# Kernel tuning notes

Measured on AMD Instinct MI355X. Metric: run time of the kernel, lower is better.

The kernel has to match this reference:

```python
import jax, jax.numpy as jnp
import numpy as np


def _block_causal_mask(cu_seqlens, seq_len):
    """Boolean [seq_len, seq_len] mask: True = attend (same doc AND causal)."""
    positions = jnp.arange(seq_len)
    # searchsorted(side='right') - 1 maps each position to its document id
    seq_ids = jnp.searchsorted(cu_seqlens, positions, side='right') - 1
    same_seq = seq_ids[:, None] == seq_ids[None, :]
    causal = positions[None, :] <= positions[:, None]
    return same_seq & causal


def setup_inputs() -> dict:
    key = jax.random.key(0)
    kq, kk, kv, kc = jax.random.split(key, 4)
    B, H, S, D = 1, 16, 4096, 128
    q = jax.random.normal(kq, (B, H, S, D), dtype=jnp.float32)
    k = jax.random.normal(kk, (B, H, S, D), dtype=jnp.float32)
    v = jax.random.normal(kv, (B, H, S, D), dtype=jnp.float32)
    # 8 packed documents: interior boundaries are sorted random ints in (0, S)
    inner = jnp.sort(jax.random.randint(kc, (7,), 1, S, dtype=jnp.int64))
    cu_seqlens = jnp.concatenate([
        jnp.zeros((1,), jnp.int64), inner, jnp.full((1,), S, jnp.int64)
    ])
    return {"q": q, "k": k, "v": v, "cu_seqlens": cu_seqlens, "max_seqlen": S}


def reference(q, k, v, cu_seqlens, max_seqlen):
    # q, k, v: [B, H, S, D]; block-diagonal causal SDPA over packed sequences.
    S, D = q.shape[2], q.shape[3]
    scale = 1.0 / jnp.sqrt(jnp.asarray(D, q.dtype))
    allow = _block_causal_mask(cu_seqlens, S)  # [S, S] bool
    scores = jnp.einsum('bhsd,bhtd->bhst', q, k) * scale  # [B, H, S, S]
    neg_inf = jnp.asarray(-jnp.inf, scores.dtype)
    scores = jnp.where(allow[None, None], scores, neg_inf)
    probs = jax.nn.softmax(scores, axis=-1)
    return jnp.einsum('bhst,bhtd->bhsd', probs, v)
```

## Files before the change

kernel.cpp:

```cpp
#include <hip/hip_runtime.h>

typedef float  f32x4  __attribute__((ext_vector_type(4)));
typedef __bf16 bf16x8 __attribute__((ext_vector_type(8)));
typedef unsigned short u16;
typedef u16 u16x8 __attribute__((ext_vector_type(8)));
typedef u16 u16x4 __attribute__((ext_vector_type(4)));

#define HEADS 16
#define DIM   128
#define QT    64
#define KTILE 64
#define PSTR  72
#define KSTR  136
#define VSTR  68

__device__ __forceinline__ u16 f2bf(float f) {
    unsigned u = __builtin_bit_cast(unsigned, f);
    u += 0x7FFFu + ((u >> 16) & 1u);
    return (u16)(u >> 16);
}

__device__ __forceinline__ void dma16(const void* g, void* l) {
    auto* gp = (const __attribute__((address_space(1))) unsigned*)(uintptr_t)g;
    auto* lp = (__attribute__((address_space(3))) unsigned*)(uintptr_t)l;
    __builtin_amdgcn_global_load_lds(gp, lp, 16, 0, 0);
}

__global__ __launch_bounds__(256) void prep_k(
    const float* __restrict__ K, u16* __restrict__ KB, int S, int total)
{
    int t = blockIdx.x * 256 + threadIdx.x;
    if (t >= total) return;
    int g = t & 15;
    int k = (t >> 4) % S;
    int h = (t >> 4) / S;
    int r = k & 63, tile = k >> 6;
    const float* src = K + ((long)(h * S + k) * DIM + g * 8);
    f32x4 a = *(const f32x4*)src;
    f32x4 b = *(const f32x4*)(src + 4);
    u16x8 o;
    o[0]=f2bf(a[0]); o[1]=f2bf(a[1]); o[2]=f2bf(a[2]); o[3]=f2bf(a[3]);
    o[4]=f2bf(b[0]); o[5]=f2bf(b[1]); o[6]=f2bf(b[2]); o[7]=f2bf(b[3]);
    long tb = (long)(h * (S >> 6) + tile) * 8192;
    *(u16x8*)&KB[tb + r * 128 + ((g ^ (r & 7)) << 3)] = o;
}

__global__ __launch_bounds__(256) void prep_v(
    const float* __restrict__ V, u16* __restrict__ VB, int S)
{
    __shared__ __align__(16) u16 T[128 * 72];
    int nt = S >> 6;
    int tile = blockIdx.x % nt, h = blockIdx.x / nt;
    int t = threadIdx.x;
    int col4 = (t & 31) * 4;
    int row  = t >> 5;
    const float* src = V + ((long)(h * S + tile * 64)) * DIM;
#pragma unroll
    for (int it = 0; it < 8; ++it) {
        int k = row + it * 8;
        f32x4 x = *(const f32x4*)(src + (long)k * DIM + col4);
        T[(col4 + 0) * 72 + k] = f2bf(x[0]);
        T[(col4 + 1) * 72 + k] = f2bf(x[1]);
        T[(col4 + 2) * 72 + k] = f2bf(x[2]);
        T[(col4 + 3) * 72 + k] = f2bf(x[3]);
    }
    __syncthreads();
    long tb = (long)(h * nt + tile) * 8192;
#pragma unroll
    for (int it = 0; it < 4; ++it) {
        int idx = t + it * 256;
        int d = idx >> 3, g2 = idx & 7;
        u16x8 o = *(const u16x8*)&T[d * 72 + g2 * 8];
        *(u16x8*)&VB[tb + d * 64 + ((g2 ^ (d & 7)) << 3)] = o;
    }
}

__global__ __launch_bounds__(256, 3) void fa_main(
    const float* __restrict__ Q, const u16* __restrict__ KB,
    const u16* __restrict__ VB, const void* __restrict__ cu_raw,
    int n_cu, float* __restrict__ O, int S, int n_qb)
{
    __shared__ __align__(16) u16 Kb[64 * 128];
    __shared__ __align__(16) u16 Vt[144 * 64];
    __shared__ __align__(16) u16 Pw[4][16 * PSTR];
    __shared__ int cu_s[32];

    const int tid  = threadIdx.x;
    const int wave = tid >> 6, lane = tid & 63;
    const int quad = lane >> 4, l16 = lane & 15;
    const int h  = blockIdx.x & (HEADS - 1);
    const int qb = (n_qb - 1) - (blockIdx.x >> 4);
    const int q0 = qb * QT;

    {
        const int* cu32 = (const int*)cu_raw;
        bool is64 = (cu32[1] == 0);
        for (int t = tid; t < n_cu; t += blockDim.x)
            cu_s[t] = is64 ? (int)((const long long*)cu_raw)[t] : cu32[t];
    }
    for (int i = tid; i < 1024; i += 256)
        Vt[8192 + i] = (i < 64) ? (u16)0x3F80 : (u16)0;
    __syncthreads();

    const float sc2 = 0.08838834764831845f * 1.4426950408889634f;
    const long hb = (long)h * S * DIM;
    const long hk = (long)h * (S >> 6) * 8192;
    const int qend = q0 + QT;

    int qstart[4];
#pragma unroll
    for (int r = 0; r < 4; ++r) {
        int qi = q0 + wave * 16 + quad * 4 + r;
        int st = 0;
        for (int j = 0; j < n_cu; ++j) if (cu_s[j] <= qi) st = cu_s[j];
        qstart[r] = st;
    }
    int q0s = 0;
    for (int j = 0; j < n_cu; ++j) if (cu_s[j] <= q0) q0s = cu_s[j];

    bf16x8 qfrag[4];
    {
        const float* qp = Q + hb + (long)(q0 + wave * 16 + l16) * DIM + quad * 8;
#pragma unroll
        for (int kk = 0; kk < 4; ++kk) {
            f32x4 x = *(const f32x4*)(qp + kk * 32);
            f32x4 y = *(const f32x4*)(qp + kk * 32 + 4);
            u16x8 u;
            u[0]=f2bf(x[0]); u[1]=f2bf(x[1]); u[2]=f2bf(x[2]); u[3]=f2bf(x[3]);
            u[4]=f2bf(y[0]); u[5]=f2bf(y[1]); u[6]=f2bf(y[2]); u[7]=f2bf(y[3]);
            qfrag[kk] = __builtin_bit_cast(bf16x8, u);
        }
    }

    f32x4 acc[9];
#pragma unroll
    for (int dt = 0; dt < 9; ++dt) acc[dt] = (f32x4){0.f, 0.f, 0.f, 0.f};

    for (int kt = q0s & ~(KTILE - 1); kt < qend; kt += KTILE) {
        __syncthreads();
        {
            const u16* ks = KB + hk + (long)(kt >> 6) * 8192;
            const u16* vs = VB + hk + (long)(kt >> 6) * 8192;
#pragma unroll
            for (int c = 0; c < 4; ++c) {
                int ch = wave * 4 + c;
                dma16(ks + ch * 512 + lane * 8, &Kb[ch * 512]);
                dma16(vs + ch * 512 + lane * 8, &Vt[ch * 512]);
            }
        }
        __syncthreads();

        f32x4 sc[4];
#pragma unroll
        for (int nt = 0; nt < 4; ++nt) sc[nt] = (f32x4){0.f, 0.f, 0.f, 0.f};
#pragma unroll
        for (int kk = 0; kk < 4; ++kk)
#pragma unroll
            for (int nt = 0; nt < 4; ++nt) {
                int row = nt * 16 + l16;
                int g = kk * 4 + quad;
                u16x8 bu = *(const u16x8*)&Kb[row * 128 + ((g ^ (row & 7)) << 3)];
                sc[nt] = __builtin_amdgcn_mfma_f32_16x16x32_bf16(
                    qfrag[kk], __builtin_bit_cast(bf16x8, bu), sc[nt], 0, 0, 0);
            }

#pragma unroll
        for (int nt = 0; nt < 4; ++nt) {
            int kj = kt + nt * 16 + l16;
#pragma unroll
            for (int r = 0; r < 4; ++r) {
                int qi = q0 + wave * 16 + quad * 4 + r;
                bool ok = (kj >= qstart[r]) && (kj <= qi);
                float pv = ok ? __builtin_amdgcn_exp2f(sc[nt][r] * sc2) : 0.f;
                Pw[wave][(quad*4 + r) * PSTR + ((nt ^ quad) * 16 + l16)] = f2bf(pv);
            }
        }

#pragma unroll
        for (int kk2 = 0; kk2 < 2; ++kk2) {
            int colx = (kk2*32 + quad*8) ^ ((l16 >> 2) << 4);
            u16x8 au = *(const u16x8*)&Pw[wave][l16 * PSTR + colx];
            bf16x8 ap = __builtin_bit_cast(bf16x8, au);
#pragma unroll
            for (int dt = 0; dt < 9; ++dt) {
                int d = dt * 16 + l16;
                int g2 = kk2 * 4 + quad;
                u16x8 bu = *(const u16x8*)&Vt[(d << 6) + ((g2 ^ (d & 7)) << 3)];
                acc[dt] = __builtin_amdgcn_mfma_f32_16x16x32_bf16(
                    ap, __builtin_bit_cast(bf16x8, bu), acc[dt], 0, 0, 0);
            }
        }
    }

#pragma unroll
    for (int r = 0; r < 4; ++r) {
        float l = __shfl(acc[8][r], (lane & 48), 64);
        int qi = q0 + wave * 16 + quad * 4 + r;
        float inv = 1.f / l;
        float* op = O + hb + (long)qi * DIM + l16;
#pragma unroll
        for (int dt = 0; dt < 8; ++dt)
            op[dt * 16] = acc[dt][r] * inv;
    }
}

__global__ __launch_bounds__(256, 2) void fa_fallback(
    const float* __restrict__ Q, const float* __restrict__ K,
    const float* __restrict__ V, const void* __restrict__ cu_raw,
    int n_cu, float* __restrict__ O, int S)
{
    __shared__ __align__(16) u16 Kb[KTILE * KSTR];
    __shared__ __align__(16) u16 Vt[DIM * VSTR];
    __shared__ __align__(16) u16 Pw[4][16 * PSTR];
    __shared__ int cu_s[32];

    const int tid  = threadIdx.x;
    const int wave = tid >> 6, lane = tid & 63;
    const int quad = lane >> 4, l16 = lane & 15;
    const int q0   = blockIdx.x * QT;
    const int h    = blockIdx.y;
    const int cg = tid & 31, rr = tid >> 5;
    const int dv = tid & 127, hiv = tid >> 7;

    {
        const int* cu32 = (const int*)cu_raw;
        bool is64 = (cu32[1] == 0);
        for (int t = tid; t < n_cu; t += blockDim.x)
            cu_s[t] = is64 ? (int)((const long long*)cu_raw)[t] : cu32[t];
    }
    __syncthreads();

    const long hb = (long)h * S * DIM;
    const float NEG_INF = -__builtin_inff();
    const float scale = 0.08838834764831845f;

    int qstart[4];
#pragma unroll
    for (int r = 0; r < 4; ++r) {
        int qi = q0 + wave * 16 + quad * 4 + r;
        int st = 0;
        for (int j = 0; j < n_cu; ++j) if (cu_s[j] <= qi) st = cu_s[j];
        qstart[r] = st;
    }
    int q0s = 0;
    for (int j = 0; j < n_cu; ++j) if (cu_s[j] <= q0) q0s = cu_s[j];

    bf16x8 qfrag[4];
    {
        const float* qp = Q + hb + (long)(q0 + wave * 16 + l16) * DIM + quad * 8;
#pragma unroll
        for (int kk = 0; kk < 4; ++kk) {
            f32x4 x = *(const f32x4*)(qp + kk * 32);
            f32x4 y = *(const f32x4*)(qp + kk * 32 + 4);
            u16x8 u;
            u[0]=f2bf(x[0]); u[1]=f2bf(x[1]); u[2]=f2bf(x[2]); u[3]=f2bf(x[3]);
            u[4]=f2bf(y[0]); u[5]=f2bf(y[1]); u[6]=f2bf(y[2]); u[7]=f2bf(y[3]);
            qfrag[kk] = __builtin_bit_cast(bf16x8, u);
        }
    }

    f32x4 acc[8];
#pragma unroll
    for (int dt = 0; dt < 8; ++dt) acc[dt] = (f32x4){0.f, 0.f, 0.f, 0.f};
    float m_r[4], l_r[4];
#pragma unroll
    for (int r = 0; r < 4; ++r) { m_r[r] = NEG_INF; l_r[r] = 0.f; }

    for (int kt = q0s & ~(KTILE - 1); kt < q0 + QT; kt += KTILE) {
        __syncthreads();
        {
#pragma unroll
            for (int it = 0; it < 8; ++it) {
                f32x4 kx = *(const f32x4*)(K + hb + (long)(kt + rr + it*8) * DIM + cg*4);
                u16x4 kb4;
                kb4[0]=f2bf(kx[0]); kb4[1]=f2bf(kx[1]);
                kb4[2]=f2bf(kx[2]); kb4[3]=f2bf(kx[3]);
                *(u16x4*)&Kb[(rr + it*8) * KSTR + cg*4] = kb4;
            }
#pragma unroll
            for (int p = 0; p < 8; ++p) {
                int kq = 2*p + hiv;
                const float* vp = V + hb + (long)(kt + kq*4) * DIM + dv;
                u16x4 w;
                w[0]=f2bf(vp[0]); w[1]=f2bf(vp[(long)DIM]);
                w[2]=f2bf(vp[(long)2*DIM]); w[3]=f2bf(vp[(long)3*DIM]);
                *(u16x4*)&Vt[dv * VSTR + kq*4] = w;
            }
        }
        __syncthreads();

        f32x4 sc[4];
#pragma unroll
        for (int nt = 0; nt < 4; ++nt) sc[nt] = (f32x4){0.f, 0.f, 0.f, 0.f};
#pragma unroll
        for (int kk = 0; kk < 4; ++kk)
#pragma unroll
            for (int nt = 0; nt < 4; ++nt) {
                u16x8 bu = *(const u16x8*)&Kb[(nt*16 + l16) * KSTR + kk*32 + quad*8];
                sc[nt] = __builtin_amdgcn_mfma_f32_16x16x32_bf16(
                    qfrag[kk], __builtin_bit_cast(bf16x8, bu), sc[nt], 0, 0, 0);
            }
#pragma unroll
        for (int nt = 0; nt < 4; ++nt) {
            int kj = kt + nt * 16 + l16;
#pragma unroll
            for (int r = 0; r < 4; ++r) {
                int qi = q0 + wave * 16 + quad * 4 + r;
                bool ok = (kj >= qstart[r]) && (kj <= qi);
                sc[nt][r] = ok ? sc[nt][r] * scale : NEG_INF;
            }
        }
        float mnew[4], alpha[4], rsum[4];
#pragma unroll
        for (int r = 0; r < 4; ++r) {
            float tm = fmaxf(fmaxf(sc[0][r], sc[1][r]), fmaxf(sc[2][r], sc[3][r]));
#pragma unroll
            for (int off = 1; off < 16; off <<= 1)
                tm = fmaxf(tm, __shfl_xor(tm, off, 64));
            float mn = fmaxf(m_r[r], tm);
            mnew[r]  = mn;
            alpha[r] = (mn == NEG_INF) ? 1.f : __expf(m_r[r] - mn);
            rsum[r]  = 0.f;
        }
#pragma unroll
        for (int nt = 0; nt < 4; ++nt)
#pragma unroll
            for (int r = 0; r < 4; ++r) {
                float pv = (sc[nt][r] == NEG_INF) ? 0.f : __expf(sc[nt][r] - mnew[r]);
                sc[nt][r] = pv;
                rsum[r] += pv;
            }
#pragma unroll
        for (int r = 0; r < 4; ++r) {
            float s = rsum[r];
#pragma unroll
            for (int off = 1; off < 16; off <<= 1) s += __shfl_xor(s, off, 64);
            l_r[r] = l_r[r] * alpha[r] + s;
            m_r[r] = mnew[r];
        }
#pragma unroll
        for (int dt = 0; dt < 8; ++dt)
#pragma unroll
            for (int r = 0; r < 4; ++r) acc[dt][r] *= alpha[r];

#pragma unroll
        for (int nt = 0; nt < 4; ++nt)
#pragma unroll
            for (int r = 0; r < 4; ++r)
                Pw[wave][(quad*4 + r) * PSTR + ((nt ^ quad) * 16 + l16)] = f2bf(sc[nt][r]);

#pragma unroll
        for (int kk2 = 0; kk2 < 2; ++kk2) {
            int colx = (kk2*32 + quad*8) ^ ((l16 >> 2) << 4);
            u16x8 au = *(const u16x8*)&Pw[wave][l16 * PSTR + colx];
            bf16x8 ap = __builtin_bit_cast(bf16x8, au);
#pragma unroll
            for (int dt = 0; dt < 8; ++dt) {
                int base = (dt*16 + l16) * VSTR + kk2*32 + quad*8;
                u16x4 lo = *(const u16x4*)&Vt[base];
                u16x4 hi = *(const u16x4*)&Vt[base + 4];
                u16x8 bu;
                bu[0]=lo[0]; bu[1]=lo[1]; bu[2]=lo[2]; bu[3]=lo[3];
                bu[4]=hi[0]; bu[5]=hi[1]; bu[6]=hi[2]; bu[7]=hi[3];
                acc[dt] = __builtin_amdgcn_mfma_f32_16x16x32_bf16(
                    ap, __builtin_bit_cast(bf16x8, bu), acc[dt], 0, 0, 0);
            }
        }
    }

#pragma unroll
    for (int r = 0; r < 4; ++r) {
        int qi = q0 + wave * 16 + quad * 4 + r;
        float inv = 1.f / l_r[r];
        float* op = O + hb + (long)qi * DIM + l16;
#pragma unroll
        for (int dt = 0; dt < 8; ++dt)
            op[dt * 16] = acc[dt][r] * inv;
    }
}

extern "C" void kernel_launch(void* const* d_in, const int* in_sizes, int n_in,
                              void* d_out, int out_size, void* d_ws, size_t ws_size,
                              hipStream_t stream) {
    const float* q = (const float*)d_in[0];
    const float* k = (const float*)d_in[1];
    const float* v = (const float*)d_in[2];
    const void* cu = d_in[3];
    int n_cu = in_sizes[3];
    int S = in_sizes[0] / (HEADS * DIM);
    size_t perMat = (size_t)HEADS * S * 256;
    if (ws_size >= 2 * perMat) {
        u16* KB = (u16*)d_ws;
        u16* VB = (u16*)((char*)d_ws + perMat);
        int totalK = HEADS * S * 16;
        prep_k<<<dim3((totalK + 255) / 256), 256, 0, stream>>>(k, KB, S, totalK);
        prep_v<<<dim3(HEADS * (S >> 6)), 256, 0, stream>>>(v, VB, S);
        int n_qb = S / QT;
        fa_main<<<dim3(n_qb * HEADS), 256, 0, stream>>>(
            q, KB, VB, cu, n_cu, (float*)d_out, S, n_qb);
    } else {
        fa_fallback<<<dim3(S / QT, HEADS), 256, 0, stream>>>(
            q, k, v, cu, n_cu, (float*)d_out, S);
    }
}
```

Measured before the change: 188.0 us.

## Double query tile per block so each wave reuses K/V fragments over two row tiles

The main kernel's query tile grows from 64 to 128 rows, with each wave now handling two 16-row M-tiles. Each K fragment and V fragment read from LDS feeds two MFMAs, which halves LDS and global K/V traffic per query row. In exchange, register pressure roughly doubles, the occupancy bound drops from 3 to 2 blocks per CU, and there are half as many blocks with coarser causal tiles, so more masked work. The fallback kernel is pinned to 64-row tiles.

```diff
diff --git a/kernel.cpp b/kernel.cpp
--- a/kernel.cpp
+++ b/kernel.cpp
@@ -8,7 +8,7 @@
 
 #define HEADS 16
 #define DIM   128
-#define QT    64
+#define QT    128
 #define KTILE 64
 #define PSTR  72
 #define KSTR  136
@@ -75,14 +75,14 @@
     }
 }
 
-__global__ __launch_bounds__(256, 3) void fa_main(
+__global__ __launch_bounds__(256, 2) void fa_main(
     const float* __restrict__ Q, const u16* __restrict__ KB,
     const u16* __restrict__ VB, const void* __restrict__ cu_raw,
     int n_cu, float* __restrict__ O, int S, int n_qb)
 {
     __shared__ __align__(16) u16 Kb[64 * 128];
     __shared__ __align__(16) u16 Vt[144 * 64];
-    __shared__ __align__(16) u16 Pw[4][16 * PSTR];
+    __shared__ __align__(16) u16 Pw[4][32 * PSTR];
     __shared__ int cu_s[32];
 
     const int tid  = threadIdx.x;
@@ -91,6 +91,7 @@
     const int h  = blockIdx.x & (HEADS - 1);
     const int qb = (n_qb - 1) - (blockIdx.x >> 4);
     const int q0 = qb * QT;
+    const int wrow = q0 + wave * 32;
 
     {
         const int* cu32 = (const int*)cu_raw;
@@ -107,20 +108,23 @@
     const long hk = (long)h * (S >> 6) * 8192;
     const int qend = q0 + QT;
 
-    int qstart[4];
-#pragma unroll
-    for (int r = 0; r < 4; ++r) {
-        int qi = q0 + wave * 16 + quad * 4 + r;
-        int st = 0;
-        for (int j = 0; j < n_cu; ++j) if (cu_s[j] <= qi) st = cu_s[j];
-        qstart[r] = st;
-    }
+    int qstart[2][4];
+#pragma unroll
+    for (int mt = 0; mt < 2; ++mt)
+#pragma unroll
+        for (int r = 0; r < 4; ++r) {
+            int qi = wrow + mt * 16 + quad * 4 + r;
+            int st = 0;
+            for (int j = 0; j < n_cu; ++j) if (cu_s[j] <= qi) st = cu_s[j];
+            qstart[mt][r] = st;
+        }
     int q0s = 0;
     for (int j = 0; j < n_cu; ++j) if (cu_s[j] <= q0) q0s = cu_s[j];
 
-    bf16x8 qfrag[4];
-    {
-        const float* qp = Q + hb + (long)(q0 + wave * 16 + l16) * DIM + quad * 8;
+    bf16x8 qfrag[2][4];
+#pragma unroll
+    for (int mt = 0; mt < 2; ++mt) {
+        const float* qp = Q + hb + (long)(wrow + mt * 16 + l16) * DIM + quad * 8;
 #pragma unroll
         for (int kk = 0; kk < 4; ++kk) {
             f32x4 x = *(const f32x4*)(qp + kk * 32);
@@ -128,13 +132,15 @@
             u16x8 u;
             u[0]=f2bf(x[0]); u[1]=f2bf(x[1]); u[2]=f2bf(x[2]); u[3]=f2bf(x[3]);
             u[4]=f2bf(y[0]); u[5]=f2bf(y[1]); u[6]=f2bf(y[2]); u[7]=f2bf(y[3]);
-            qfrag[kk] = __builtin_bit_cast(bf16x8, u);
-        }
-    }
-
-    f32x4 acc[9];
-#pragma unroll
-    for (int dt = 0; dt < 9; ++dt) acc[dt] = (f32x4){0.f, 0.f, 0.f, 0.f};
+            qfrag[mt][kk] = __builtin_bit_cast(bf16x8, u);
+        }
+    }
+
+    f32x4 acc[2][9];
+#pragma unroll
+    for (int mt = 0; mt < 2; ++mt)
+#pragma unroll
+        for (int dt = 0; dt < 9; ++dt) acc[mt][dt] = (f32x4){0.f, 0.f, 0.f, 0.f};
 
     for (int kt = q0s & ~(KTILE - 1); kt < qend; kt += KTILE) {
         __syncthreads();
@@ -150,9 +156,11 @@
         }
         __syncthreads();
 
-        f32x4 sc[4];
-#pragma unroll
-        for (int nt = 0; nt < 4; ++nt) sc[nt] = (f32x4){0.f, 0.f, 0.f, 0.f};
+        f32x4 sc[2][4];
+#pragma unroll
+        for (int mt = 0; mt < 2; ++mt)
+#pragma unroll
+            for (int nt = 0; nt < 4; ++nt) sc[mt][nt] = (f32x4){0.f, 0.f, 0.f, 0.f};
 #pragma unroll
         for (int kk = 0; kk < 4; ++kk)
 #pragma unroll
@@ -160,48 +168,61 @@
                 int row = nt * 16 + l16;
                 int g = kk * 4 + quad;
                 u16x8 bu = *(const u16x8*)&Kb[row * 128 + ((g ^ (row & 7)) << 3)];
-                sc[nt] = __builtin_amdgcn_mfma_f32_16x16x32_bf16(
-                    qfrag[kk], __builtin_bit_cast(bf16x8, bu), sc[nt], 0, 0, 0);
-            }
-
-#pragma unroll
-        for (int nt = 0; nt < 4; ++nt) {
-            int kj = kt + nt * 16 + l16;
-#pragma unroll
-            for (int r = 0; r < 4; ++r) {
-                int qi = q0 + wave * 16 + quad * 4 + r;
-                bool ok = (kj >= qstart[r]) && (kj <= qi);
-                float pv = ok ? __builtin_amdgcn_exp2f(sc[nt][r] * sc2) : 0.f;
-                Pw[wave][(quad*4 + r) * PSTR + ((nt ^ quad) * 16 + l16)] = f2bf(pv);
-            }
-        }
+                bf16x8 bf = __builtin_bit_cast(bf16x8, bu);
+                sc[0][nt] = __builtin_amdgcn_mfma_f32_16x16x32_bf16(
+                    qfrag[0][kk], bf, sc[0][nt], 0, 0, 0);
+                sc[1][nt] = __builtin_amdgcn_mfma_f32_16x16x32_bf16(
+                    qfrag[1][kk], bf, sc[1][nt], 0, 0, 0);
+            }
+
+#pragma unroll
+        for (int mt = 0; mt < 2; ++mt)
+#pragma unroll
+            for (int nt = 0; nt < 4; ++nt) {
+                int kj = kt + nt * 16 + l16;
+#pragma unroll
+                for (int r = 0; r < 4; ++r) {
+                    int qi = wrow + mt * 16 + quad * 4 + r;
+                    bool ok = (kj >= qstart[mt][r]) && (kj <= qi);
+                    float pv = ok ? __builtin_amdgcn_exp2f(sc[mt][nt][r] * sc2) : 0.f;
+                    Pw[wave][(mt*16 + quad*4 + r) * PSTR + ((nt ^ quad) * 16 + l16)]
+                        = f2bf(pv);
+                }
+            }
 
 #pragma unroll
         for (int kk2 = 0; kk2 < 2; ++kk2) {
             int colx = (kk2*32 + quad*8) ^ ((l16 >> 2) << 4);
-            u16x8 au = *(const u16x8*)&Pw[wave][l16 * PSTR + colx];
-            bf16x8 ap = __builtin_bit_cast(bf16x8, au);
+            bf16x8 ap0 = __builtin_bit_cast(bf16x8,
+                *(const u16x8*)&Pw[wave][l16 * PSTR + colx]);
+            bf16x8 ap1 = __builtin_bit_cast(bf16x8,
+                *(const u16x8*)&Pw[wave][(16 + l16) * PSTR + colx]);
 #pragma unroll
             for (int dt = 0; dt < 9; ++dt) {
                 int d = dt * 16 + l16;
                 int g2 = kk2 * 4 + quad;
                 u16x8 bu = *(const u16x8*)&Vt[(d << 6) + ((g2 ^ (d & 7)) << 3)];
-                acc[dt] = __builtin_amdgcn_mfma_f32_16x16x32_bf16(
-                    ap, __builtin_bit_cast(bf16x8, bu), acc[dt], 0, 0, 0);
-            }
-        }
-    }
-
-#pragma unroll
-    for (int r = 0; r < 4; ++r) {
-        float l = __shfl(acc[8][r], (lane & 48), 64);
-        int qi = q0 + wave * 16 + quad * 4 + r;
-        float inv = 1.f / l;
-        float* op = O + hb + (long)qi * DIM + l16;
-#pragma unroll
-        for (int dt = 0; dt < 8; ++dt)
-            op[dt * 16] = acc[dt][r] * inv;
-    }
+                bf16x8 bf = __builtin_bit_cast(bf16x8, bu);
+                acc[0][dt] = __builtin_amdgcn_mfma_f32_16x16x32_bf16(
+                    ap0, bf, acc[0][dt], 0, 0, 0);
+                acc[1][dt] = __builtin_amdgcn_mfma_f32_16x16x32_bf16(
+                    ap1, bf, acc[1][dt], 0, 0, 0);
+            }
+        }
+    }
+
+#pragma unroll
+    for (int mt = 0; mt < 2; ++mt)
+#pragma unroll
+        for (int r = 0; r < 4; ++r) {
+            float l = __shfl(acc[mt][8][r], (lane & 48), 64);
+            int qi = wrow + mt * 16 + quad * 4 + r;
+            float inv = 1.f / l;
+            float* op = O + hb + (long)qi * DIM + l16;
+#pragma unroll
+            for (int dt = 0; dt < 8; ++dt)
+                op[dt * 16] = acc[mt][dt][r] * inv;
+        }
 }
 
 __global__ __launch_bounds__(256, 2) void fa_fallback(
@@ -217,7 +238,7 @@
     const int tid  = threadIdx.x;
     const int wave = tid >> 6, lane = tid & 63;
     const int quad = lane >> 4, l16 = lane & 15;
-    const int q0   = blockIdx.x * QT;
+    const int q0   = blockIdx.x * 64;
     const int h    = blockIdx.y;
     const int cg = tid & 31, rr = tid >> 5;
     const int dv = tid & 127, hiv = tid >> 7;
@@ -266,7 +287,7 @@
 #pragma unroll
     for (int r = 0; r < 4; ++r) { m_r[r] = NEG_INF; l_r[r] = 0.f; }
 
-    for (int kt = q0s & ~(KTILE - 1); kt < q0 + QT; kt += KTILE) {
+    for (int kt = q0s & ~(KTILE - 1); kt < q0 + 64; kt += KTILE) {
         __syncthreads();
         {
 #pragma unroll
@@ -389,7 +410,7 @@
     int n_cu = in_sizes[3];
     int S = in_sizes[0] / (HEADS * DIM);
     size_t perMat = (size_t)HEADS * S * 256;
-    if (ws_size >= 2 * perMat) {
+    if (ws_size >= 2 * perMat && (S % QT) == 0) {
         u16* KB = (u16*)d_ws;
         u16* VB = (u16*)((char*)d_ws + perMat);
         int totalK = HEADS * S * 16;
@@ -399,7 +420,7 @@
         fa_main<<<dim3(n_qb * HEADS), 256, 0, stream>>>(
             q, KB, VB, cu, n_cu, (float*)d_out, S, n_qb);
     } else {
-        fa_fallback<<<dim3(S / QT, HEADS), 256, 0, stream>>>(
+        fa_fallback<<<dim3(S / 64, HEADS), 256, 0, stream>>>(
             q, k, v, cu, n_cu, (float*)d_out, S);
     }
 }
```

Result: slower. 205.1 us (+9.1%).
